# Optimization experiments

Hardware: AMD Instinct MI355X
Metric: run time of the kernel (lower is better)

## Reference

```python
import jax, jax.numpy as jnp
import numpy as np

# ---- ANI symmetry-function constants (from __init__ defaults) ----
N_ATOMS = 50000
N_ELEMENTS = 7
RADIAL_CUTOFF = 5.1      # angstrom
ANGULAR_CUTOFF = 3.5     # angstrom
RADIAL_START = 0.8
ANGULAR_START = 0.8
RADIAL_DIV = 8           # radial_sublength = 8
ANGULAR_DIV = 8
ANGLE_SECTIONS = 4       # angular sublength = 4*8 = 32
ETA_R = 19.7
ETA_A = 12.5
ZETA = 14.1

ShfR = np.linspace(RADIAL_START, RADIAL_CUTOFF, RADIAL_DIV + 1, dtype=np.float32)[:-1]
ShfA = np.linspace(ANGULAR_START, ANGULAR_CUTOFF, ANGULAR_DIV + 1, dtype=np.float32)[:-1]
ShfZ = ((np.arange(ANGLE_SECTIONS, dtype=np.float32) + 0.5) * np.pi / ANGLE_SECTIONS)


def cosine_cutoff(d, rc):
    return jnp.where(d <= rc, 0.5 * jnp.cos(jnp.pi * d / rc) + 0.5, 0.0)


def setup_inputs() -> dict:
    key = jax.random.key(0)
    k1, k2, k3, k4, k5 = jax.random.split(key, 5)
    n_pairs, n_trip = 1_600_000, 1_600_000
    # pair distances in [0.8, 5.1)
    r_ij = jax.random.uniform(k1, (n_pairs,), jnp.float32) * (RADIAL_CUTOFF - RADIAL_START) + RADIAL_START
    pair_indices = jax.random.randint(k2, (2, n_pairs), 0, N_ATOMS, jnp.int32)
    atomic_numbers = jax.random.randint(k3, (N_ATOMS,), 0, N_ELEMENTS, jnp.int32)
    # triplet displacement vectors with norms in [0.8, 3.5)
    dirs = jax.random.normal(k4, (2, n_trip, 3), jnp.float32)
    dirs = dirs / jnp.linalg.norm(dirs, axis=-1, keepdims=True)
    mags = jax.random.uniform(k5, (2, n_trip, 1), jnp.float32) * (ANGULAR_CUTOFF - ANGULAR_START) + ANGULAR_START
    vec12 = dirs * mags
    return {"r_ij": r_ij, "pair_indices": pair_indices,
            "atomic_numbers": atomic_numbers, "vec12": vec12}


def _radial_features(d):
    # [P, 8]: ANI radial symmetry function
    fc = cosine_cutoff(d, RADIAL_CUTOFF)
    g = 0.25 * jnp.exp(-ETA_R * (d[:, None] - jnp.asarray(ShfR)) ** 2)
    return g * fc[:, None]


def _angular_features(vec12):
    v1, v2 = vec12[0], vec12[1]                       # [T, 3]
    d1 = jnp.linalg.norm(v1, axis=-1)
    d2 = jnp.linalg.norm(v2, axis=-1)
    cos_t = 0.95 * jnp.sum(v1 * v2, axis=-1) / (d1 * d2)
    theta = jnp.arccos(cos_t)                         # [T]
    f_ang = ((1.0 + jnp.cos(theta[:, None] - jnp.asarray(ShfZ))) * 0.5) ** ZETA   # [T, 4]
    f_rad = jnp.exp(-ETA_A * (0.5 * (d1 + d2)[:, None] - jnp.asarray(ShfA)) ** 2) # [T, 8]
    fc = cosine_cutoff(d1, ANGULAR_CUTOFF) * cosine_cutoff(d2, ANGULAR_CUTOFF)    # [T]
    ang = 2.0 * f_ang[:, :, None] * f_rad[:, None, :] * fc[:, None, None]          # [T, 4, 8]
    return ang.reshape(ang.shape[0], ANGLE_SECTIONS * ANGULAR_DIV)                 # [T, 32]


def reference(r_ij, pair_indices, atomic_numbers, vec12):
    # radial branch
    feat = _radial_features(r_ij)                     # [P, 8]
    species12 = atomic_numbers[pair_indices]          # [2, P]
    index12 = pair_indices * N_ELEMENTS + species12[::-1]  # flip(0): use partner species
    aev = jnp.zeros((N_ATOMS * N_ELEMENTS, RADIAL_DIV), feat.dtype)
    aev = aev.at[index12[0]].add(feat).at[index12[1]].add(feat)
    # angular branch
    ang = _angular_features(vec12)                    # [T, 32]
    return (aev, ang)
```

## Files before the change

kernel.cpp:

```cpp
#include <hip/hip_runtime.h>


#define N_ATOMS 50000
#define N_ELEM 7
#define RADIAL_DIV 8
#define NROWS (N_ATOMS * N_ELEM)

constexpr float RADIAL_CUTOFF = 5.1f;
constexpr float ANGULAR_CUTOFF = 3.5f;
constexpr float ETA_R = 19.7f;
constexpr float ETA_A = 12.5f;
constexpr float ZETA = 14.1f;
constexpr float PI_F = 3.14159265358979323846f;
constexpr float FP_SCALE = 4096.0f;
constexpr float FP_INV = 1.0f / 4096.0f;
constexpr float SHELL_STEP = 0.5375f;
constexpr float INV_SHELL_STEP = 1.0f / 0.5375f;

__device__ __constant__ float CSZ[4] = { 0.9238795325f,  0.3826834324f, -0.3826834324f, -0.9238795325f };
__device__ __constant__ float SNZ[4] = { 0.3826834324f,  0.9238795325f,  0.9238795325f,  0.3826834324f };

__global__ void radial_kernel(const float* __restrict__ r_ij,
                              const int* __restrict__ pair_idx,
                              const int* __restrict__ Z,
                              unsigned long long* __restrict__ acc,
                              int P) {
    int t = blockIdx.x * blockDim.x + threadIdx.x;
    if (t >= P) return;
    float d = r_ij[t];
    float fc = (d <= RADIAL_CUTOFF) ? (0.5f * __cosf(PI_F * d * (1.0f / RADIAL_CUTOFF)) + 0.5f) : 0.0f;

    float x = (d - 0.8f) * INV_SHELL_STEP;
    int k0 = (int)(x + 0.5f);
    k0 = min(max(k0, 1), 6);
    int a = k0 - 1;
    int g = a >> 1;
    int sh = (a & 1) << 4;

    unsigned long long w = 0ull;
    #pragma unroll
    for (int j = 0; j < 3; j++) {
        float diff = d - (0.8f + SHELL_STEP * (float)(a + j));
        float gv = 0.25f * __expf(-ETA_R * diff * diff) * fc;
        unsigned int q = (unsigned int)(gv * FP_SCALE + 0.5f);
        w |= (unsigned long long)q << (16 * j);
    }
    w <<= sh;
    if (w == 0ull) return;

    int i0 = pair_idx[t];
    int i1 = pair_idx[P + t];
    int s0 = Z[i0];
    int s1 = Z[i1];
    atomicAdd(acc + ((size_t)i0 * N_ELEM + s1) * 3 + g, w);
    atomicAdd(acc + ((size_t)i1 * N_ELEM + s0) * 3 + g, w);
}

__global__ void convert_kernel(const unsigned long long* __restrict__ acc,
                               float* __restrict__ aev, int nrows) {
    int r = blockIdx.x * blockDim.x + threadIdx.x;
    if (r >= nrows) return;
    unsigned long long g0 = acc[3 * (size_t)r + 0];
    unsigned long long g1 = acc[3 * (size_t)r + 1];
    unsigned long long g2 = acc[3 * (size_t)r + 2];
    unsigned int l0[4], l1[4], l2[4];
    #pragma unroll
    for (int j = 0; j < 4; j++) {
        l0[j] = (unsigned int)(g0 >> (16 * j)) & 0xFFFFu;
        l1[j] = (unsigned int)(g1 >> (16 * j)) & 0xFFFFu;
        l2[j] = (unsigned int)(g2 >> (16 * j)) & 0xFFFFu;
    }
    float4 oa, ob;
    oa.x = (float)(l0[0])         * FP_INV;
    oa.y = (float)(l0[1])         * FP_INV;
    oa.z = (float)(l0[2] + l1[0]) * FP_INV;
    oa.w = (float)(l0[3] + l1[1]) * FP_INV;
    ob.x = (float)(l1[2] + l2[0]) * FP_INV;
    ob.y = (float)(l1[3] + l2[1]) * FP_INV;
    ob.z = (float)(l2[2])         * FP_INV;
    ob.w = (float)(l2[3])         * FP_INV;
    float4* o = reinterpret_cast<float4*>(aev + 8ull * (size_t)r);
    o[0] = oa;
    o[1] = ob;
}

#define ABLK 256
__global__ void angular_kernel(const float* __restrict__ vec12,
                               float* __restrict__ ang,
                               int T) {
    __shared__ float sm[ABLK * 33];
    int tid = threadIdx.x;
    int t = blockIdx.x * ABLK + tid;

    float vals[32];
    if (t < T) {
        const float* v1 = vec12 + 3ull * (size_t)t;
        const float* v2 = vec12 + 3ull * (size_t)T + 3ull * (size_t)t;
        float x1 = v1[0], y1 = v1[1], z1 = v1[2];
        float x2 = v2[0], y2 = v2[1], z2 = v2[2];

        float d1 = sqrtf(x1 * x1 + y1 * y1 + z1 * z1);
        float d2 = sqrtf(x2 * x2 + y2 * y2 + z2 * z2);
        float dot = x1 * x2 + y1 * y2 + z1 * z2;
        float cost = 0.95f * dot / (d1 * d2);
        float sint = sqrtf(fmaxf(0.0f, 1.0f - cost * cost));

        float fc1 = (d1 <= ANGULAR_CUTOFF) ? (0.5f * __cosf(PI_F * d1 * (1.0f / ANGULAR_CUTOFF)) + 0.5f) : 0.0f;
        float fc2 = (d2 <= ANGULAR_CUTOFF) ? (0.5f * __cosf(PI_F * d2 * (1.0f / ANGULAR_CUTOFF)) + 0.5f) : 0.0f;
        float fc = fc1 * fc2;

        float davg = 0.5f * (d1 + d2);
        float frad[8];
        #pragma unroll
        for (int k = 0; k < 8; k++) {
            float diff = davg - (0.8f + 0.3375f * (float)k);
            frad[k] = __expf(-ETA_A * diff * diff);
        }
        #pragma unroll
        for (int j = 0; j < 4; j++) {
            float c = 0.5f * (1.0f + cost * CSZ[j] + sint * SNZ[j]);
            float base = 2.0f * __powf(c, ZETA) * fc;
            #pragma unroll
            for (int k = 0; k < 8; k++) vals[j * 8 + k] = base * frad[k];
        }
    } else {
        #pragma unroll
        for (int k = 0; k < 32; k++) vals[k] = 0.0f;
    }

    #pragma unroll
    for (int k = 0; k < 32; k++) sm[tid * 33 + k] = vals[k];
    __syncthreads();

    size_t base = (size_t)blockIdx.x * ABLK * 32;
    size_t lim = (size_t)T * 32;
    #pragma unroll
    for (int it = 0; it < 8; it++) {
        int f = it * ABLK + tid;
        int row = f >> 3;
        int col = (f & 7) * 4;
        float4 o;
        o.x = sm[row * 33 + col + 0];
        o.y = sm[row * 33 + col + 1];
        o.z = sm[row * 33 + col + 2];
        o.w = sm[row * 33 + col + 3];
        size_t gidx = base + (size_t)f * 4;
        if (gidx < lim) reinterpret_cast<float4*>(ang)[gidx >> 2] = o;
    }
}

extern "C" void kernel_launch(void* const* d_in, const int* in_sizes, int n_in,
                              void* d_out, int out_size, void* d_ws, size_t ws_size,
                              hipStream_t stream) {
    const float* r_ij     = (const float*)d_in[0];
    const int*   pair_idx = (const int*)d_in[1];
    const int*   Z        = (const int*)d_in[2];
    const float* vec12    = (const float*)d_in[3];

    const int P = in_sizes[0];
    const int T = in_sizes[3] / 6;

    float* aev = (float*)d_out;
    float* ang = aev + (size_t)NROWS * RADIAL_DIV;

    unsigned long long* acc = (unsigned long long*)d_ws;
    hipMemsetAsync(acc, 0, (size_t)NROWS * 3 * sizeof(unsigned long long), stream);

    radial_kernel<<<dim3((P + 255) / 256), dim3(256), 0, stream>>>(r_ij, pair_idx, Z, acc, P);
    convert_kernel<<<dim3((NROWS + 255) / 256), dim3(256), 0, stream>>>(acc, aev, NROWS);
    angular_kernel<<<dim3((T + ABLK - 1) / ABLK), dim3(ABLK), 0, stream>>>(vec12, ang, T);
}
```

Before: 398.1 us.

## Fuse radial scatter and angular kernels into one interleaved launch

```diff
diff --git a/kernel.cpp b/kernel.cpp
--- a/kernel.cpp
+++ b/kernel.cpp
@@ -20,78 +20,69 @@
 __device__ __constant__ float CSZ[4] = { 0.9238795325f,  0.3826834324f, -0.3826834324f, -0.9238795325f };
 __device__ __constant__ float SNZ[4] = { 0.3826834324f,  0.9238795325f,  0.9238795325f,  0.3826834324f };
 
-__global__ void radial_kernel(const float* __restrict__ r_ij,
-                              const int* __restrict__ pair_idx,
-                              const int* __restrict__ Z,
-                              unsigned long long* __restrict__ acc,
-                              int P) {
-    int t = blockIdx.x * blockDim.x + threadIdx.x;
-    if (t >= P) return;
-    float d = r_ij[t];
-    float fc = (d <= RADIAL_CUTOFF) ? (0.5f * __cosf(PI_F * d * (1.0f / RADIAL_CUTOFF)) + 0.5f) : 0.0f;
+#define BLK 256
 
-    float x = (d - 0.8f) * INV_SHELL_STEP;
-    int k0 = (int)(x + 0.5f);
-    k0 = min(max(k0, 1), 6);
-    int a = k0 - 1;
-    int g = a >> 1;
-    int sh = (a & 1) << 4;
+__global__ __launch_bounds__(BLK) void fused_kernel(
+        const float* __restrict__ r_ij,
+        const int* __restrict__ pair_idx,
+        const int* __restrict__ Z,
+        unsigned long long* __restrict__ acc,
+        int P,
+        const float* __restrict__ vec12,
+        float* __restrict__ ang,
+        int T,
+        int nRad, int nAng) {
+    __shared__ float sm[BLK * 33];
+    int bid = blockIdx.x;
+    int tid = threadIdx.x;
 
-    unsigned long long w = 0ull;
-    #pragma unroll
-    for (int j = 0; j < 3; j++) {
-        float diff = d - (0.8f + SHELL_STEP * (float)(a + j));
-        float gv = 0.25f * __expf(-ETA_R * diff * diff) * fc;
-        unsigned int q = (unsigned int)(gv * FP_SCALE + 0.5f);
-        w |= (unsigned long long)q << (16 * j);
+    int paired = min(nRad, nAng);
+    bool isAng;
+    int id;
+    if (bid < 2 * paired) {
+        isAng = ((bid & 1) == 0);
+        id = bid >> 1;
+    } else {
+        id = bid - paired;
+        isAng = (nAng > nRad);
     }
-    w <<= sh;
-    if (w == 0ull) return;
 
-    int i0 = pair_idx[t];
-    int i1 = pair_idx[P + t];
-    int s0 = Z[i0];
-    int s1 = Z[i1];
-    atomicAdd(acc + ((size_t)i0 * N_ELEM + s1) * 3 + g, w);
-    atomicAdd(acc + ((size_t)i1 * N_ELEM + s0) * 3 + g, w);
-}
+    if (!isAng) {
+        int t = id * BLK + tid;
+        if (t >= P) return;
+        float d = r_ij[t];
+        float fc = (d <= RADIAL_CUTOFF)
+                       ? (0.5f * __cosf(PI_F * d * (1.0f / RADIAL_CUTOFF)) + 0.5f)
+                       : 0.0f;
 
-__global__ void convert_kernel(const unsigned long long* __restrict__ acc,
-                               float* __restrict__ aev, int nrows) {
-    int r = blockIdx.x * blockDim.x + threadIdx.x;
-    if (r >= nrows) return;
-    unsigned long long g0 = acc[3 * (size_t)r + 0];
-    unsigned long long g1 = acc[3 * (size_t)r + 1];
-    unsigned long long g2 = acc[3 * (size_t)r + 2];
-    unsigned int l0[4], l1[4], l2[4];
-    #pragma unroll
-    for (int j = 0; j < 4; j++) {
-        l0[j] = (unsigned int)(g0 >> (16 * j)) & 0xFFFFu;
-        l1[j] = (unsigned int)(g1 >> (16 * j)) & 0xFFFFu;
-        l2[j] = (unsigned int)(g2 >> (16 * j)) & 0xFFFFu;
+        float x = (d - 0.8f) * INV_SHELL_STEP;
+        int k0 = (int)(x + 0.5f);
+        k0 = min(max(k0, 1), 6);
+        int a = k0 - 1;
+        int g = a >> 1;
+        int sh = (a & 1) << 4;
+
+        unsigned long long w = 0ull;
+        #pragma unroll
+        for (int j = 0; j < 3; j++) {
+            float diff = d - (0.8f + SHELL_STEP * (float)(a + j));
+            float gv = 0.25f * __expf(-ETA_R * diff * diff) * fc;
+            unsigned int q = (unsigned int)(gv * FP_SCALE + 0.5f);
+            w |= (unsigned long long)q << (16 * j);
+        }
+        w <<= sh;
+        if (w == 0ull) return;
+
+        int i0 = pair_idx[t];
+        int i1 = pair_idx[P + t];
+        int s0 = Z[i0];
+        int s1 = Z[i1];
+        atomicAdd(acc + ((size_t)i0 * N_ELEM + s1) * 3 + g, w);
+        atomicAdd(acc + ((size_t)i1 * N_ELEM + s0) * 3 + g, w);
+        return;
     }
-    float4 oa, ob;
-    oa.x = (float)(l0[0])         * FP_INV;
-    oa.y = (float)(l0[1])         * FP_INV;
-    oa.z = (float)(l0[2] + l1[0]) * FP_INV;
-    oa.w = (float)(l0[3] + l1[1]) * FP_INV;
-    ob.x = (float)(l1[2] + l2[0]) * FP_INV;
-    ob.y = (float)(l1[3] + l2[1]) * FP_INV;
-    ob.z = (float)(l2[2])         * FP_INV;
-    ob.w = (float)(l2[3])         * FP_INV;
-    float4* o = reinterpret_cast<float4*>(aev + 8ull * (size_t)r);
-    o[0] = oa;
-    o[1] = ob;
-}
 
-#define ABLK 256
-__global__ void angular_kernel(const float* __restrict__ vec12,
-                               float* __restrict__ ang,
-                               int T) {
-    __shared__ float sm[ABLK * 33];
-    int tid = threadIdx.x;
-    int t = blockIdx.x * ABLK + tid;
-
+    int t = id * BLK + tid;
     float vals[32];
     if (t < T) {
         const float* v1 = vec12 + 3ull * (size_t)t;
@@ -132,11 +123,11 @@
     for (int k = 0; k < 32; k++) sm[tid * 33 + k] = vals[k];
     __syncthreads();
 
-    size_t base = (size_t)blockIdx.x * ABLK * 32;
+    size_t base = (size_t)id * BLK * 32;
     size_t lim = (size_t)T * 32;
     #pragma unroll
     for (int it = 0; it < 8; it++) {
-        int f = it * ABLK + tid;
+        int f = it * BLK + tid;
         int row = f >> 3;
         int col = (f & 7) * 4;
         float4 o;
@@ -147,6 +138,34 @@
         size_t gidx = base + (size_t)f * 4;
         if (gidx < lim) reinterpret_cast<float4*>(ang)[gidx >> 2] = o;
     }
+}
+
+__global__ void convert_kernel(const unsigned long long* __restrict__ acc,
+                               float* __restrict__ aev, int nrows) {
+    int r = blockIdx.x * blockDim.x + threadIdx.x;
+    if (r >= nrows) return;
+    unsigned long long g0 = acc[3 * (size_t)r + 0];
+    unsigned long long g1 = acc[3 * (size_t)r + 1];
+    unsigned long long g2 = acc[3 * (size_t)r + 2];
+    unsigned int l0[4], l1[4], l2[4];
+    #pragma unroll
+    for (int j = 0; j < 4; j++) {
+        l0[j] = (unsigned int)(g0 >> (16 * j)) & 0xFFFFu;
+        l1[j] = (unsigned int)(g1 >> (16 * j)) & 0xFFFFu;
+        l2[j] = (unsigned int)(g2 >> (16 * j)) & 0xFFFFu;
+    }
+    float4 oa, ob;
+    oa.x = (float)(l0[0])         * FP_INV;
+    oa.y = (float)(l0[1])         * FP_INV;
+    oa.z = (float)(l0[2] + l1[0]) * FP_INV;
+    oa.w = (float)(l0[3] + l1[1]) * FP_INV;
+    ob.x = (float)(l1[2] + l2[0]) * FP_INV;
+    ob.y = (float)(l1[3] + l2[1]) * FP_INV;
+    ob.z = (float)(l2[2])         * FP_INV;
+    ob.w = (float)(l2[3])         * FP_INV;
+    float4* o = reinterpret_cast<float4*>(aev + 8ull * (size_t)r);
+    o[0] = oa;
+    o[1] = ob;
 }
 
 extern "C" void kernel_launch(void* const* d_in, const int* in_sizes, int n_in,
@@ -166,7 +185,9 @@
     unsigned long long* acc = (unsigned long long*)d_ws;
     hipMemsetAsync(acc, 0, (size_t)NROWS * 3 * sizeof(unsigned long long), stream);
 
-    radial_kernel<<<dim3((P + 255) / 256), dim3(256), 0, stream>>>(r_ij, pair_idx, Z, acc, P);
+    const int nRad = (P + BLK - 1) / BLK;
+    const int nAng = (T + BLK - 1) / BLK;
+    fused_kernel<<<dim3(nRad + nAng), dim3(BLK), 0, stream>>>(
+        r_ij, pair_idx, Z, acc, P, vec12, ang, T, nRad, nAng);
     convert_kernel<<<dim3((NROWS + 255) / 256), dim3(256), 0, stream>>>(acc, aev, NROWS);
-    angular_kernel<<<dim3((T + ABLK - 1) / ABLK), dim3(ABLK), 0, stream>>>(vec12, ang, T);
 }
```

Measured after the change: 369.7 us. 7.1% less time.
